# Performance work log

Measured on AMD Instinct MI355X. Metric: run time of the kernel, lower is better.

## Reference

```python
import jax, jax.numpy as jnp
import numpy as np

# Fixed by JastrowNet source: ElectronicSchNet(n_interactions=2, kernel_dim=8, embedding_dim=16, version=1)
BATCH = 512
N_UP, N_DOWN = 16, 16
N_ELEC = N_UP + N_DOWN
N_ATOMS = 8
DIST_FEAT = 32
KERNEL = 8
EMBED = 16
N_LAYERS = 2
W_HIDDEN = 16  # log-spaced hidden dim of the w filter MLP: round(sqrt(32*8))
N_CHAN = 3     # same-spin, anti-spin, nuclear filter channels


def ssp(x):
    # shifted softplus used by SchNet
    return jax.nn.softplus(x) - jnp.log(2.0).astype(x.dtype)


def setup_inputs() -> dict:
    key = jax.random.key(0)
    ks = jax.random.split(key, 16)
    s = lambda fan_in: 1.0 / np.sqrt(fan_in)
    inp = {
        # Gaussian-expanded distance features are non-negative
        'edges_elec': jax.random.uniform(ks[0], (BATCH, N_ELEC, N_ELEC, DIST_FEAT), jnp.float32),
        'edges_nuc': jax.random.uniform(ks[1], (BATCH, N_ELEC, N_ATOMS, DIST_FEAT), jnp.float32),
        # electron spin embedding table (up=0, down=1) and nuclear embeddings Y
        'X_emb': jax.random.normal(ks[2], (2, EMBED), jnp.float32),
        'Y': jax.random.normal(ks[3], (N_ATOMS, KERNEL), jnp.float32),
        # per-layer, per-channel w filter MLP (dist_feat -> hidden -> kernel)
        'wW1': jax.random.normal(ks[4], (N_LAYERS, N_CHAN, DIST_FEAT, W_HIDDEN), jnp.float32) * s(DIST_FEAT),
        'wb1': jnp.zeros((N_LAYERS, N_CHAN, W_HIDDEN), jnp.float32),
        'wW2': jax.random.normal(ks[5], (N_LAYERS, N_CHAN, W_HIDDEN, KERNEL), jnp.float32) * s(W_HIDDEN),
        'wb2': jnp.zeros((N_LAYERS, N_CHAN, KERNEL), jnp.float32),
        # per-layer h subnet (embed -> kernel) and g subnet (kernel -> embed)
        'hW': jax.random.normal(ks[6], (N_LAYERS, EMBED, KERNEL), jnp.float32) * s(EMBED),
        'hb': jnp.zeros((N_LAYERS, KERNEL), jnp.float32),
        'gW': jax.random.normal(ks[7], (N_LAYERS, KERNEL, EMBED), jnp.float32) * s(KERNEL),
        'gb': jnp.zeros((N_LAYERS, EMBED), jnp.float32),
        # readout: Linear(16, 1, bias=False)
        'orb_W': jax.random.normal(ks[8], (EMBED,), jnp.float32) * s(EMBED),
    }
    return inp


def reference(edges_elec, edges_nuc, X_emb, Y, wW1, wb1, wW2, wb2, hW, hb, gW, gb, orb_W):
    B = edges_elec.shape[0]
    spins = jnp.concatenate([jnp.zeros(N_UP, jnp.int32), jnp.ones(N_DOWN, jnp.int32)])
    not_self = ~jnp.eye(N_ELEC, dtype=bool)
    same = ((spins[:, None] == spins[None, :]) & not_self)  # [n,n]
    anti = (spins[:, None] != spins[None, :])

    # initial electron embeddings by spin, broadcast over batch
    x = jnp.broadcast_to(X_emb[spins], (B, N_ELEC, EMBED))

    for l in range(N_LAYERS):
        def w_sub(e, c):
            h1 = ssp(e @ wW1[l, c] + wb1[l, c])
            return ssp(h1 @ wW2[l, c] + wb2[l, c])  # [..., KERNEL]

        w_same = w_sub(edges_elec, 0) * same[None, :, :, None]  # [B,n,n,k]
        w_anti = w_sub(edges_elec, 1) * anti[None, :, :, None]
        w_n = w_sub(edges_nuc, 2)                                # [B,n,m,k]

        hx = ssp(x @ hW[l] + hb[l])                              # [B,n,k]
        # continuous-filter message passing: gather neighbor features, multiply by filter, scatter-sum
        z = jnp.einsum('bijk,bjk->bik', w_same + w_anti, hx)
        z = z + jnp.einsum('bimk,mk->bik', w_n, Y)
        # version 1: single g applied to combined message, residual update
        x = x + z @ gW[l] + gb[l]

    # orbital readout Linear(16,1,bias=False).squeeze(-1).sum(-1)
    return (x @ orb_W).sum(axis=-1)  # [B]
```

## Files before the change

### kernel.cpp

```cpp
#include <hip/hip_runtime.h>
#include <hip/hip_bf16.h>
#include <cstddef>
#include <cstdint>


#define NB   512
#define NE   32
#define NA   8
#define NF   32
#define NH   16
#define NK   8
#define NEMB 16

typedef __attribute__((ext_vector_type(8))) short short8;
typedef __attribute__((ext_vector_type(4))) float f32x4;

__device__ __forceinline__ float ssp(float v){
    return fmaxf(v, 0.f) + __logf(1.f + __expf(-fabsf(v))) - 0.6931471805599453f;
}

__device__ __forceinline__ short f2bf(float x){
    unsigned b = __float_as_uint(x);
    b += 0x7fffu + ((b >> 16) & 1u);
    return (short)(b >> 16);
}
__device__ __forceinline__ unsigned packbf2(float lo, float hi){
    return (unsigned)(unsigned short)f2bf(lo) | ((unsigned)(unsigned short)f2bf(hi) << 16);
}

extern "C" __global__ void __launch_bounds__(256, 4)
filters_kernel(const float* __restrict__ edges_elec,
               const float* __restrict__ edges_nuc,
               const float* __restrict__ X_emb,
               const float* __restrict__ Yk,
               const float* __restrict__ wW1, const float* __restrict__ wb1,
               const float* __restrict__ wW2, const float* __restrict__ wb2,
               const float* __restrict__ hW,  const float* __restrict__ hb,
               __hip_bfloat16* __restrict__ w2out,
               float* __restrict__ z1p,
               float* __restrict__ zn1, float* __restrict__ zn2)
{
    const int bid = blockIdx.x, t = threadIdx.x;
    const int p = bid >> 9, b = bid & 511;
    const bool isNuc = (p == 4);
    const int qi = p >> 1, qj = p & 1;
    const int cc = isNuc ? 2 : ((qi == qj) ? 0 : 1);

    const int lane = t & 63;
    const int r16 = lane & 15, g4 = lane >> 4;
    const int wq = (t >> 6) * 4;

    short8 a1[2], a2[2];
    f32x4 c1[2], c2[2];
#pragma unroll
    for (int l = 0; l < 2; l++){
        const float* W1 = wW1 + (size_t)(l*3 + cc)*NF*NH;
        const float* W2 = wW2 + (size_t)(l*3 + cc)*NH*NK;
        short8 s, s2;
#pragma unroll
        for (int e = 0; e < 8; e++){
            s[e] = f2bf(W1[(g4*8 + e)*NH + r16]);
            const int h = g4*8 + e;
            s2[e] = (h < NH && r16 < NK) ? f2bf(W2[h*NK + r16]) : (short)0;
        }
        a1[l] = s;
        a2[l] = s2;
        const float* B1 = wb1 + (l*3 + cc)*NH;
        const float* B2 = wb2 + (l*3 + cc)*NK;
        f32x4 cb1, cb2;
#pragma unroll
        for (int r = 0; r < 4; r++){
            const int m = g4*4 + r;
            cb1[r] = B1[m];
            cb2[r] = (m < NK) ? B2[m] : 0.f;
        }
        c1[l] = cb1; c2[l] = cb2;
    }

    float hx[4] = {0.f,0.f,0.f,0.f};
    float Yv[4] = {0.f,0.f,0.f,0.f};
    if (!isNuc){
#pragma unroll
        for (int r = 0; r < 4; r++){
            const int kk = (g4*4 + r) & 7;
            float acc = hb[kk];
#pragma unroll
            for (int e = 0; e < NEMB; e++)
                acc = fmaf(X_emb[qj*NEMB + e], hW[e*NK + kk], acc);
            hx[r] = ssp(acc);
        }
    } else {
        const int m = lane & 7;
#pragma unroll
        for (int r = 0; r < 4; r++)
            Yv[r] = Yk[m*NK + ((g4*4 + r) & 7)];
    }

    float4 rawA[4], rawB[4];
    if (!isNuc){
#pragma unroll
        for (int g = 0; g < 4; g++){
            const int i = qi*16 + wq + g;
            const float* src = edges_elec + (((size_t)b*NE + i)*NE + (qj*16 + r16))*NF + g4*8;
            rawA[g] = ((const float4*)src)[0];
            rawB[g] = ((const float4*)src)[1];
        }
    } else {
#pragma unroll
        for (int g = 0; g < 4; g++){
            const int gp = wq + g;
            const int i = 2*gp + (r16 >> 3), m = r16 & 7;
            const float* src = edges_nuc + (((size_t)b*NE + i)*NA + m)*NF + g4*8;
            rawA[g] = ((const float4*)src)[0];
            rawB[g] = ((const float4*)src)[1];
        }
    }
    short8 bfr[4];
#pragma unroll
    for (int g = 0; g < 4; g++){
        short8 s;
        s[0]=f2bf(rawA[g].x); s[1]=f2bf(rawA[g].y); s[2]=f2bf(rawA[g].z); s[3]=f2bf(rawA[g].w);
        s[4]=f2bf(rawB[g].x); s[5]=f2bf(rawB[g].y); s[6]=f2bf(rawB[g].z); s[7]=f2bf(rawB[g].w);
        bfr[g] = s;
    }

    const int s0 = (g4*32 + r16) & 63;
    const int s1 = (g4*32 + 16 + r16) & 63;

#pragma unroll
    for (int g = 0; g < 4; g++){
#pragma unroll
        for (int l = 0; l < 2; l++){
            f32x4 d1 = __builtin_amdgcn_mfma_f32_16x16x32_bf16(a1[l], bfr[g], c1[l], 0, 0, 0);
            const unsigned p0 = packbf2(ssp(d1[0]), ssp(d1[1]));
            const unsigned p1 = packbf2(ssp(d1[2]), ssp(d1[3]));
            unsigned q0 = __shfl(p0, s0, 64);
            unsigned q1 = __shfl(p1, s0, 64);
            unsigned q2 = __shfl(p0, s1, 64);
            unsigned q3 = __shfl(p1, s1, 64);
            if (g4 >= 2){ q0 = 0u; q1 = 0u; q2 = 0u; q3 = 0u; }
            union { unsigned u[4]; short8 v; } bb;
            bb.u[0]=q0; bb.u[1]=q1; bb.u[2]=q2; bb.u[3]=q3;
            f32x4 d2 = __builtin_amdgcn_mfma_f32_16x16x32_bf16(a2[l], bb.v, c2[l], 0, 0, 0);
            float wk[4];
#pragma unroll
            for (int r = 0; r < 4; r++) wk[r] = ssp(d2[r]);

            if (!isNuc){
                const int i16 = wq + g;
                if (cc == 0 && r16 == i16){
#pragma unroll
                    for (int r = 0; r < 4; r++) wk[r] = 0.f;
                }
                if (l == 0){
#pragma unroll
                    for (int off = 1; off < 16; off <<= 1)
#pragma unroll
                        for (int r = 0; r < 4; r++) wk[r] += __shfl_xor(wk[r], off, 64);
                    if (r16 == 0 && g4 < 2){
                        const int i = qi*16 + i16;
                        float4 st;
                        st.x = wk[0]*hx[0]; st.y = wk[1]*hx[1];
                        st.z = wk[2]*hx[2]; st.w = wk[3]*hx[3];
                        *(float4*)&z1p[(((size_t)b*2 + qj)*NE + i)*NK + g4*4] = st;
                    }
                } else if (g4 < 2){
                    const int i = qi*16 + i16, j = qj*16 + r16;
                    uint2 uu;
                    uu.x = packbf2(wk[0], wk[1]);
                    uu.y = packbf2(wk[2], wk[3]);
                    *(uint2*)&w2out[(((size_t)b*NE + i)*NE + j)*NK + g4*4] = uu;
                }
            } else {
#pragma unroll
                for (int r = 0; r < 4; r++) wk[r] *= Yv[r];
#pragma unroll
                for (int off = 1; off < 8; off <<= 1)
#pragma unroll
                    for (int r = 0; r < 4; r++) wk[r] += __shfl_xor(wk[r], off, 64);
                if ((r16 & 7) == 0 && g4 < 2){
                    const int i = 2*(wq + g) + (r16 >> 3);
                    float* dst = (l == 0) ? zn1 : zn2;
                    float4 st; st.x = wk[0]; st.y = wk[1]; st.z = wk[2]; st.w = wk[3];
                    *(float4*)&dst[((size_t)b*NE + i)*NK + g4*4] = st;
                }
            }
        }
    }
}

extern "C" __global__ void __launch_bounds__(256, 4)
update_kernel(const float* __restrict__ X_emb,
              const float* __restrict__ hW,  const float* __restrict__ hb,
              const float* __restrict__ gW,  const float* __restrict__ gb,
              const float* __restrict__ orbW,
              const __hip_bfloat16* __restrict__ w2,
              const float* __restrict__ z1p,
              const float* __restrict__ zn1, const float* __restrict__ zn2,
              float* __restrict__ out)
{
    __shared__ float s_x[NE*NEMB];
    __shared__ float s_z[NE*NK];
    __shared__ float s_hx[NE*NK];
    __shared__ float s_gW[2*NK*NEMB];
    __shared__ float s_gb[2*NEMB];
    __shared__ float s_hW1[NEMB*NK];
    __shared__ float s_hb1[NK];
    __shared__ float s_orb[NEMB];
    __shared__ float s_red[4];

    const int b = blockIdx.x, t = threadIdx.x;

    s_gW[t] = gW[t];
    if (t < 2*NEMB)  s_gb[t]  = gb[t];
    if (t < NEMB*NK) s_hW1[t] = hW[NEMB*NK + t];
    if (t < NK)      s_hb1[t] = hb[NK + t];
    if (t < NEMB)    s_orb[t] = orbW[t];
    {
        const int i = t >> 3, k = t & 7;
        s_z[t] = z1p[(((size_t)b*2 + 0)*NE + i)*NK + k]
               + z1p[(((size_t)b*2 + 1)*NE + i)*NK + k]
               + zn1[((size_t)b*NE + i)*NK + k];
    }
    __syncthreads();
#pragma unroll
    for (int q = 0; q < 2; q++){
        const int idx = q*256 + t, i = idx >> 4, e = idx & 15;
        float acc = s_gb[e];
#pragma unroll
        for (int k = 0; k < NK; k++)
            acc = fmaf(s_z[i*NK + k], s_gW[k*NEMB + e], acc);
        s_x[idx] = X_emb[(i >> 4)*NEMB + e] + acc;
    }
    __syncthreads();
    {
        const int i = t >> 3, k = t & 7;
        float acc = s_hb1[k];
#pragma unroll
        for (int e = 0; e < NEMB; e++)
            acc = fmaf(s_x[i*NEMB + e], s_hW1[e*NK + k], acc);
        s_hx[t] = ssp(acc);
    }
    __syncthreads();
    {
        const int i16 = t >> 4, j16 = t & 15;
#pragma unroll
        for (int qh = 0; qh < 2; qh++){
            const int i = qh*16 + i16;
            float zacc[NK];
#pragma unroll
            for (int k = 0; k < NK; k++) zacc[k] = 0.f;
#pragma unroll
            for (int qj = 0; qj < 2; qj++){
                const int j = qj*16 + j16;
                union { uint4 u; __hip_bfloat16 h[8]; } raw;
                raw.u = *(const uint4*)&w2[((size_t)b*NE*NE + i*NE + j)*NK];
                float pk[NK];
#pragma unroll
                for (int k = 0; k < NK; k++)
                    pk[k] = __bfloat162float(raw.h[k]) * s_hx[j*NK + k];
#pragma unroll
                for (int off = 8; off > 0; off >>= 1)
#pragma unroll
                    for (int k = 0; k < NK; k++) pk[k] += __shfl_down(pk[k], off, 16);
#pragma unroll
                for (int k = 0; k < NK; k++) zacc[k] += pk[k];
            }
            if (j16 == 0){
#pragma unroll
                for (int k = 0; k < NK; k++) s_z[i*NK + k] = zacc[k];
            }
        }
    }
    __syncthreads();
    { const int i = t >> 3, k = t & 7; s_z[t] += zn2[((size_t)b*NE + i)*NK + k]; }
    __syncthreads();
#pragma unroll
    for (int q = 0; q < 2; q++){
        const int idx = q*256 + t, i = idx >> 4, e = idx & 15;
        float acc = s_gb[NEMB + e];
#pragma unroll
        for (int k = 0; k < NK; k++)
            acc = fmaf(s_z[i*NK + k], s_gW[NK*NEMB + k*NEMB + e], acc);
        s_x[idx] += acc;
    }
    __syncthreads();
    float part = (s_x[t] + s_x[t + 256]) * s_orb[t & 15];
#pragma unroll
    for (int off = 32; off > 0; off >>= 1) part += __shfl_down(part, off, 64);
    if ((t & 63) == 0) s_red[t >> 6] = part;
    __syncthreads();
    if (t == 0) out[b] = s_red[0] + s_red[1] + s_red[2] + s_red[3];
}

extern "C" void kernel_launch(void* const* d_in, const int* in_sizes, int n_in,
                              void* d_out, int out_size, void* d_ws, size_t ws_size,
                              hipStream_t stream)
{
    const float* edges_elec = (const float*)d_in[0];
    const float* edges_nuc  = (const float*)d_in[1];
    const float* X_emb      = (const float*)d_in[2];
    const float* Yk         = (const float*)d_in[3];
    const float* wW1        = (const float*)d_in[4];
    const float* wb1        = (const float*)d_in[5];
    const float* wW2        = (const float*)d_in[6];
    const float* wb2        = (const float*)d_in[7];
    const float* hW         = (const float*)d_in[8];
    const float* hb         = (const float*)d_in[9];
    const float* gW         = (const float*)d_in[10];
    const float* gb         = (const float*)d_in[11];
    const float* orbW       = (const float*)d_in[12];

    char* ws = (char*)d_ws;
    __hip_bfloat16* w2 = (__hip_bfloat16*)ws;
    float* z1p = (float*)(ws + 8388608);
    float* zn1 = (float*)(ws + 8388608 + 1048576);
    float* zn2 = (float*)(ws + 8388608 + 1048576 + 524288);

    filters_kernel<<<5*NB, 256, 0, stream>>>(
        edges_elec, edges_nuc, X_emb, Yk, wW1, wb1, wW2, wb2, hW, hb,
        w2, z1p, zn1, zn2);
    update_kernel<<<NB, 256, 0, stream>>>(
        X_emb, hW, hb, gW, gb, orbW, w2, z1p, zn1, zn2, (float*)d_out);
}
```

Baseline: 156.5 us.

## Fuse filter and update kernels into one per-batch kernel using shared memory

Merges the two launches into a single 512-thread block per batch element. The block computes the elec and nuclear filters, keeps the layer-2 bf16 filter tile and the partial messages in LDS, then runs the residual updates and readout. This removes the global workspace round trip for the w2 filter tensor and the second launch. In exchange there are only 512 blocks, each with more serial work and about 24KB of LDS, so there is less parallelism for hiding the latency of the edge loads.

```diff
diff --git a/kernel.cpp b/kernel.cpp
--- a/kernel.cpp
+++ b/kernel.cpp
@@ -27,128 +27,111 @@
 __device__ __forceinline__ unsigned packbf2(float lo, float hi){
     return (unsigned)(unsigned short)f2bf(lo) | ((unsigned)(unsigned short)f2bf(hi) << 16);
 }
-
-extern "C" __global__ void __launch_bounds__(256, 4)
-filters_kernel(const float* __restrict__ edges_elec,
+__device__ __forceinline__ short8 cvt_row(float4 a, float4 b){
+    short8 s;
+    s[0]=f2bf(a.x); s[1]=f2bf(a.y); s[2]=f2bf(a.z); s[3]=f2bf(a.w);
+    s[4]=f2bf(b.x); s[5]=f2bf(b.y); s[6]=f2bf(b.z); s[7]=f2bf(b.w);
+    return s;
+}
+
+extern "C" __global__ void __launch_bounds__(512, 4)
+jastrow_kernel(const float* __restrict__ edges_elec,
                const float* __restrict__ edges_nuc,
                const float* __restrict__ X_emb,
                const float* __restrict__ Yk,
                const float* __restrict__ wW1, const float* __restrict__ wb1,
                const float* __restrict__ wW2, const float* __restrict__ wb2,
                const float* __restrict__ hW,  const float* __restrict__ hb,
-               __hip_bfloat16* __restrict__ w2out,
-               float* __restrict__ z1p,
-               float* __restrict__ zn1, float* __restrict__ zn2)
+               const float* __restrict__ gW,  const float* __restrict__ gb,
+               const float* __restrict__ orbW,
+               float* __restrict__ out)
 {
-    const int bid = blockIdx.x, t = threadIdx.x;
-    const int p = bid >> 9, b = bid & 511;
-    const bool isNuc = (p == 4);
-    const int qi = p >> 1, qj = p & 1;
-    const int cc = isNuc ? 2 : ((qi == qj) ? 0 : 1);
-
-    const int lane = t & 63;
+    __shared__ __align__(16) __hip_bfloat16 s_w2[NE*NE*NK];
+    __shared__ __align__(16) float s_z1p[2*NE*NK];
+    __shared__ __align__(16) float s_zn1[NE*NK];
+    __shared__ __align__(16) float s_zn2[NE*NK];
+    __shared__ float s_hx1[2*NK];
+    __shared__ float s_x[NE*NEMB];
+    __shared__ float s_z[NE*NK];
+    __shared__ float s_hx[NE*NK];
+    __shared__ float s_red[8];
+
+    const int b = blockIdx.x, t = threadIdx.x;
+    const int wid = t >> 6, lane = t & 63;
     const int r16 = lane & 15, g4 = lane >> 4;
-    const int wq = (t >> 6) * 4;
-
-    short8 a1[2], a2[2];
-    f32x4 c1[2], c2[2];
-#pragma unroll
-    for (int l = 0; l < 2; l++){
-        const float* W1 = wW1 + (size_t)(l*3 + cc)*NF*NH;
-        const float* W2 = wW2 + (size_t)(l*3 + cc)*NH*NK;
-        short8 s, s2;
-#pragma unroll
-        for (int e = 0; e < 8; e++){
-            s[e] = f2bf(W1[(g4*8 + e)*NH + r16]);
-            const int h = g4*8 + e;
-            s2[e] = (h < NH && r16 < NK) ? f2bf(W2[h*NK + r16]) : (short)0;
-        }
-        a1[l] = s;
-        a2[l] = s2;
-        const float* B1 = wb1 + (l*3 + cc)*NH;
-        const float* B2 = wb2 + (l*3 + cc)*NK;
-        f32x4 cb1, cb2;
-#pragma unroll
-        for (int r = 0; r < 4; r++){
-            const int m = g4*4 + r;
-            cb1[r] = B1[m];
-            cb2[r] = (m < NK) ? B2[m] : 0.f;
-        }
-        c1[l] = cb1; c2[l] = cb2;
-    }
-
-    float hx[4] = {0.f,0.f,0.f,0.f};
-    float Yv[4] = {0.f,0.f,0.f,0.f};
-    if (!isNuc){
-#pragma unroll
-        for (int r = 0; r < 4; r++){
-            const int kk = (g4*4 + r) & 7;
-            float acc = hb[kk];
-#pragma unroll
-            for (int e = 0; e < NEMB; e++)
-                acc = fmaf(X_emb[qj*NEMB + e], hW[e*NK + kk], acc);
-            hx[r] = ssp(acc);
-        }
-    } else {
-        const int m = lane & 7;
-#pragma unroll
-        for (int r = 0; r < 4; r++)
-            Yv[r] = Yk[m*NK + ((g4*4 + r) & 7)];
-    }
-
-    float4 rawA[4], rawB[4];
-    if (!isNuc){
-#pragma unroll
-        for (int g = 0; g < 4; g++){
-            const int i = qi*16 + wq + g;
-            const float* src = edges_elec + (((size_t)b*NE + i)*NE + (qj*16 + r16))*NF + g4*8;
-            rawA[g] = ((const float4*)src)[0];
-            rawB[g] = ((const float4*)src)[1];
-        }
-    } else {
-#pragma unroll
-        for (int g = 0; g < 4; g++){
-            const int gp = wq + g;
-            const int i = 2*gp + (r16 >> 3), m = r16 & 7;
-            const float* src = edges_nuc + (((size_t)b*NE + i)*NA + m)*NF + g4*8;
-            rawA[g] = ((const float4*)src)[0];
-            rawB[g] = ((const float4*)src)[1];
-        }
-    }
-    short8 bfr[4];
-#pragma unroll
-    for (int g = 0; g < 4; g++){
-        short8 s;
-        s[0]=f2bf(rawA[g].x); s[1]=f2bf(rawA[g].y); s[2]=f2bf(rawA[g].z); s[3]=f2bf(rawA[g].w);
-        s[4]=f2bf(rawB[g].x); s[5]=f2bf(rawB[g].y); s[6]=f2bf(rawB[g].z); s[7]=f2bf(rawB[g].w);
-        bfr[g] = s;
-    }
+
+    if (t < 2*NK){
+        const int s = t >> 3, k = t & 7;
+        float acc = hb[k];
+#pragma unroll
+        for (int e = 0; e < NEMB; e++)
+            acc = fmaf(X_emb[s*NEMB + e], hW[e*NK + k], acc);
+        s_hx1[t] = ssp(acc);
+    }
+    __syncthreads();
 
     const int s0 = (g4*32 + r16) & 63;
     const int s1 = (g4*32 + 16 + r16) & 63;
 
-#pragma unroll
-    for (int g = 0; g < 4; g++){
+    auto build = [&](int cc, short8* a1, short8* a2, f32x4* c1, f32x4* c2){
 #pragma unroll
         for (int l = 0; l < 2; l++){
-            f32x4 d1 = __builtin_amdgcn_mfma_f32_16x16x32_bf16(a1[l], bfr[g], c1[l], 0, 0, 0);
-            const unsigned p0 = packbf2(ssp(d1[0]), ssp(d1[1]));
-            const unsigned p1 = packbf2(ssp(d1[2]), ssp(d1[3]));
-            unsigned q0 = __shfl(p0, s0, 64);
-            unsigned q1 = __shfl(p1, s0, 64);
-            unsigned q2 = __shfl(p0, s1, 64);
-            unsigned q3 = __shfl(p1, s1, 64);
-            if (g4 >= 2){ q0 = 0u; q1 = 0u; q2 = 0u; q3 = 0u; }
-            union { unsigned u[4]; short8 v; } bb;
-            bb.u[0]=q0; bb.u[1]=q1; bb.u[2]=q2; bb.u[3]=q3;
-            f32x4 d2 = __builtin_amdgcn_mfma_f32_16x16x32_bf16(a2[l], bb.v, c2[l], 0, 0, 0);
-            float wk[4];
-#pragma unroll
-            for (int r = 0; r < 4; r++) wk[r] = ssp(d2[r]);
-
-            if (!isNuc){
-                const int i16 = wq + g;
-                if (cc == 0 && r16 == i16){
+            const float* W1 = wW1 + (size_t)(l*3 + cc)*NF*NH;
+            const float* W2 = wW2 + (size_t)(l*3 + cc)*NH*NK;
+            short8 s, s2;
+#pragma unroll
+            for (int e = 0; e < 8; e++){
+                s[e] = f2bf(W1[(g4*8 + e)*NH + r16]);
+                const int h = g4*8 + e;
+                s2[e] = (h < NH && r16 < NK) ? f2bf(W2[h*NK + r16]) : (short)0;
+            }
+            a1[l] = s; a2[l] = s2;
+            const float* B1 = wb1 + (l*3 + cc)*NH;
+            const float* B2 = wb2 + (l*3 + cc)*NK;
+            f32x4 cb1, cb2;
+#pragma unroll
+            for (int r = 0; r < 4; r++){
+                const int m = g4*4 + r;
+                cb1[r] = B1[m];
+                cb2[r] = (m < NK) ? B2[m] : 0.f;
+            }
+            c1[l] = cb1; c2[l] = cb2;
+        }
+    };
+
+#pragma unroll
+    for (int cc = 0; cc < 2; cc++){
+        short8 a1[2], a2[2]; f32x4 c1[2], c2[2];
+        build(cc, a1, a2, c1, c2);
+#pragma unroll
+        for (int u = 0; u < 4; u++){
+            const int tau = wid*4 + u;
+            const int qi = tau >> 4;
+            const int qj = cc ? (1 - qi) : qi;
+            const int g  = tau & 15;
+            const int i  = qi*16 + g;
+            const float* src = edges_elec
+                + (((size_t)b*NE + i)*NE + qj*16 + r16)*NF + g4*8;
+            const float4 ra = ((const float4*)src)[0];
+            const float4 rb = ((const float4*)src)[1];
+            const short8 bfr = cvt_row(ra, rb);
+#pragma unroll
+            for (int l = 0; l < 2; l++){
+                f32x4 d1 = __builtin_amdgcn_mfma_f32_16x16x32_bf16(a1[l], bfr, c1[l], 0, 0, 0);
+                const unsigned p0 = packbf2(ssp(d1[0]), ssp(d1[1]));
+                const unsigned p1 = packbf2(ssp(d1[2]), ssp(d1[3]));
+                unsigned q0 = __shfl(p0, s0, 64);
+                unsigned q1 = __shfl(p1, s0, 64);
+                unsigned q2 = __shfl(p0, s1, 64);
+                unsigned q3 = __shfl(p1, s1, 64);
+                if (g4 >= 2){ q0 = 0u; q1 = 0u; q2 = 0u; q3 = 0u; }
+                union { unsigned u4[4]; short8 v; } bb;
+                bb.u4[0]=q0; bb.u4[1]=q1; bb.u4[2]=q2; bb.u4[3]=q3;
+                f32x4 d2 = __builtin_amdgcn_mfma_f32_16x16x32_bf16(a2[l], bb.v, c2[l], 0, 0, 0);
+                float wk[4];
+#pragma unroll
+                for (int r = 0; r < 4; r++) wk[r] = ssp(d2[r]);
+                if (cc == 0 && r16 == g){
 #pragma unroll
                     for (int r = 0; r < 4; r++) wk[r] = 0.f;
                 }
@@ -158,139 +141,140 @@
 #pragma unroll
                         for (int r = 0; r < 4; r++) wk[r] += __shfl_xor(wk[r], off, 64);
                     if (r16 == 0 && g4 < 2){
-                        const int i = qi*16 + i16;
                         float4 st;
-                        st.x = wk[0]*hx[0]; st.y = wk[1]*hx[1];
-                        st.z = wk[2]*hx[2]; st.w = wk[3]*hx[3];
-                        *(float4*)&z1p[(((size_t)b*2 + qj)*NE + i)*NK + g4*4] = st;
+                        st.x = wk[0]*s_hx1[qj*NK + g4*4 + 0];
+                        st.y = wk[1]*s_hx1[qj*NK + g4*4 + 1];
+                        st.z = wk[2]*s_hx1[qj*NK + g4*4 + 2];
+                        st.w = wk[3]*s_hx1[qj*NK + g4*4 + 3];
+                        *(float4*)&s_z1p[(qj*NE + i)*NK + g4*4] = st;
                     }
                 } else if (g4 < 2){
-                    const int i = qi*16 + i16, j = qj*16 + r16;
+                    const int j = qj*16 + r16;
                     uint2 uu;
                     uu.x = packbf2(wk[0], wk[1]);
                     uu.y = packbf2(wk[2], wk[3]);
-                    *(uint2*)&w2out[(((size_t)b*NE + i)*NE + j)*NK + g4*4] = uu;
+                    *(uint2*)&s_w2[(i*NE + j)*NK + g4*4] = uu;
                 }
-            } else {
-#pragma unroll
-                for (int r = 0; r < 4; r++) wk[r] *= Yv[r];
+            }
+        }
+    }
+
+    {
+        short8 a1[2], a2[2]; f32x4 c1[2], c2[2];
+        build(2, a1, a2, c1, c2);
+        const int m = lane & 7;
+        float Yv[4];
+#pragma unroll
+        for (int r = 0; r < 4; r++)
+            Yv[r] = Yk[m*NK + ((g4*4 + r) & 7)];
+#pragma unroll
+        for (int u = 0; u < 2; u++){
+            const int gp = wid*2 + u;
+            const int i  = 2*gp + (r16 >> 3);
+            const float* src = edges_nuc
+                + (((size_t)b*NE + i)*NA + m)*NF + g4*8;
+            const float4 ra = ((const float4*)src)[0];
+            const float4 rb = ((const float4*)src)[1];
+            const short8 bfr = cvt_row(ra, rb);
+#pragma unroll
+            for (int l = 0; l < 2; l++){
+                f32x4 d1 = __builtin_amdgcn_mfma_f32_16x16x32_bf16(a1[l], bfr, c1[l], 0, 0, 0);
+                const unsigned p0 = packbf2(ssp(d1[0]), ssp(d1[1]));
+                const unsigned p1 = packbf2(ssp(d1[2]), ssp(d1[3]));
+                unsigned q0 = __shfl(p0, s0, 64);
+                unsigned q1 = __shfl(p1, s0, 64);
+                unsigned q2 = __shfl(p0, s1, 64);
+                unsigned q3 = __shfl(p1, s1, 64);
+                if (g4 >= 2){ q0 = 0u; q1 = 0u; q2 = 0u; q3 = 0u; }
+                union { unsigned u4[4]; short8 v; } bb;
+                bb.u4[0]=q0; bb.u4[1]=q1; bb.u4[2]=q2; bb.u4[3]=q3;
+                f32x4 d2 = __builtin_amdgcn_mfma_f32_16x16x32_bf16(a2[l], bb.v, c2[l], 0, 0, 0);
+                float wk[4];
+#pragma unroll
+                for (int r = 0; r < 4; r++) wk[r] = ssp(d2[r]) * Yv[r];
 #pragma unroll
                 for (int off = 1; off < 8; off <<= 1)
 #pragma unroll
                     for (int r = 0; r < 4; r++) wk[r] += __shfl_xor(wk[r], off, 64);
                 if ((r16 & 7) == 0 && g4 < 2){
-                    const int i = 2*(wq + g) + (r16 >> 3);
-                    float* dst = (l == 0) ? zn1 : zn2;
+                    float* dst = l ? s_zn2 : s_zn1;
                     float4 st; st.x = wk[0]; st.y = wk[1]; st.z = wk[2]; st.w = wk[3];
-                    *(float4*)&dst[((size_t)b*NE + i)*NK + g4*4] = st;
+                    *(float4*)&dst[i*NK + g4*4] = st;
                 }
             }
         }
     }
-}
-
-extern "C" __global__ void __launch_bounds__(256, 4)
-update_kernel(const float* __restrict__ X_emb,
-              const float* __restrict__ hW,  const float* __restrict__ hb,
-              const float* __restrict__ gW,  const float* __restrict__ gb,
-              const float* __restrict__ orbW,
-              const __hip_bfloat16* __restrict__ w2,
-              const float* __restrict__ z1p,
-              const float* __restrict__ zn1, const float* __restrict__ zn2,
-              float* __restrict__ out)
-{
-    __shared__ float s_x[NE*NEMB];
-    __shared__ float s_z[NE*NK];
-    __shared__ float s_hx[NE*NK];
-    __shared__ float s_gW[2*NK*NEMB];
-    __shared__ float s_gb[2*NEMB];
-    __shared__ float s_hW1[NEMB*NK];
-    __shared__ float s_hb1[NK];
-    __shared__ float s_orb[NEMB];
-    __shared__ float s_red[4];
-
-    const int b = blockIdx.x, t = threadIdx.x;
-
-    s_gW[t] = gW[t];
-    if (t < 2*NEMB)  s_gb[t]  = gb[t];
-    if (t < NEMB*NK) s_hW1[t] = hW[NEMB*NK + t];
-    if (t < NK)      s_hb1[t] = hb[NK + t];
-    if (t < NEMB)    s_orb[t] = orbW[t];
+    __syncthreads();
+
+    if (t < NE*NK)
+        s_z[t] = s_z1p[t] + s_z1p[NE*NK + t] + s_zn1[t];
+    __syncthreads();
     {
+        const int i = t >> 4, e = t & 15;
+        float acc = gb[e];
+#pragma unroll
+        for (int k = 0; k < NK; k++)
+            acc = fmaf(s_z[i*NK + k], gW[k*NEMB + e], acc);
+        s_x[t] = X_emb[(i >> 4)*NEMB + e] + acc;
+    }
+    __syncthreads();
+    if (t < NE*NK){
         const int i = t >> 3, k = t & 7;
-        s_z[t] = z1p[(((size_t)b*2 + 0)*NE + i)*NK + k]
-               + z1p[(((size_t)b*2 + 1)*NE + i)*NK + k]
-               + zn1[((size_t)b*NE + i)*NK + k];
-    }
-    __syncthreads();
-#pragma unroll
-    for (int q = 0; q < 2; q++){
-        const int idx = q*256 + t, i = idx >> 4, e = idx & 15;
-        float acc = s_gb[e];
+        float acc = hb[NK + k];
+#pragma unroll
+        for (int e = 0; e < NEMB; e++)
+            acc = fmaf(s_x[i*NEMB + e], hW[NEMB*NK + e*NK + k], acc);
+        s_hx[t] = ssp(acc);
+    }
+    __syncthreads();
+    {
+        const int i = t >> 4, j16 = t & 15;
+        float zacc[NK];
+#pragma unroll
+        for (int k = 0; k < NK; k++) zacc[k] = 0.f;
+#pragma unroll
+        for (int qj = 0; qj < 2; qj++){
+            const int j = qj*16 + j16;
+            union { uint4 u; __hip_bfloat16 h[8]; } raw;
+            raw.u = *(const uint4*)&s_w2[((size_t)i*NE + j)*NK];
+            float pk[NK];
+#pragma unroll
+            for (int k = 0; k < NK; k++)
+                pk[k] = __bfloat162float(raw.h[k]) * s_hx[j*NK + k];
+#pragma unroll
+            for (int off = 8; off > 0; off >>= 1)
+#pragma unroll
+                for (int k = 0; k < NK; k++) pk[k] += __shfl_down(pk[k], off, 16);
+#pragma unroll
+            for (int k = 0; k < NK; k++) zacc[k] += pk[k];
+        }
+        if (j16 == 0){
+#pragma unroll
+            for (int k = 0; k < NK; k++)
+                s_z[i*NK + k] = zacc[k] + s_zn2[i*NK + k];
+        }
+    }
+    __syncthreads();
+    {
+        const int i = t >> 4, e = t & 15;
+        float acc = gb[NEMB + e];
 #pragma unroll
         for (int k = 0; k < NK; k++)
-            acc = fmaf(s_z[i*NK + k], s_gW[k*NEMB + e], acc);
-        s_x[idx] = X_emb[(i >> 4)*NEMB + e] + acc;
-    }
-    __syncthreads();
-    {
-        const int i = t >> 3, k = t & 7;
-        float acc = s_hb1[k];
-#pragma unroll
-        for (int e = 0; e < NEMB; e++)
-            acc = fmaf(s_x[i*NEMB + e], s_hW1[e*NK + k], acc);
-        s_hx[t] = ssp(acc);
-    }
-    __syncthreads();
-    {
-        const int i16 = t >> 4, j16 = t & 15;
-#pragma unroll
-        for (int qh = 0; qh < 2; qh++){
-            const int i = qh*16 + i16;
-            float zacc[NK];
-#pragma unroll
-            for (int k = 0; k < NK; k++) zacc[k] = 0.f;
-#pragma unroll
-            for (int qj = 0; qj < 2; qj++){
-                const int j = qj*16 + j16;
-                union { uint4 u; __hip_bfloat16 h[8]; } raw;
-                raw.u = *(const uint4*)&w2[((size_t)b*NE*NE + i*NE + j)*NK];
-                float pk[NK];
-#pragma unroll
-                for (int k = 0; k < NK; k++)
-                    pk[k] = __bfloat162float(raw.h[k]) * s_hx[j*NK + k];
-#pragma unroll
-                for (int off = 8; off > 0; off >>= 1)
-#pragma unroll
-                    for (int k = 0; k < NK; k++) pk[k] += __shfl_down(pk[k], off, 16);
-#pragma unroll
-                for (int k = 0; k < NK; k++) zacc[k] += pk[k];
-            }
-            if (j16 == 0){
-#pragma unroll
-                for (int k = 0; k < NK; k++) s_z[i*NK + k] = zacc[k];
-            }
-        }
-    }
-    __syncthreads();
-    { const int i = t >> 3, k = t & 7; s_z[t] += zn2[((size_t)b*NE + i)*NK + k]; }
-    __syncthreads();
-#pragma unroll
-    for (int q = 0; q < 2; q++){
-        const int idx = q*256 + t, i = idx >> 4, e = idx & 15;
-        float acc = s_gb[NEMB + e];
-#pragma unroll
-        for (int k = 0; k < NK; k++)
-            acc = fmaf(s_z[i*NK + k], s_gW[NK*NEMB + k*NEMB + e], acc);
-        s_x[idx] += acc;
-    }
-    __syncthreads();
-    float part = (s_x[t] + s_x[t + 256]) * s_orb[t & 15];
+            acc = fmaf(s_z[i*NK + k], gW[NK*NEMB + k*NEMB + e], acc);
+        s_x[t] += acc;
+    }
+    __syncthreads();
+    float part = s_x[t] * orbW[t & 15];
 #pragma unroll
     for (int off = 32; off > 0; off >>= 1) part += __shfl_down(part, off, 64);
-    if ((t & 63) == 0) s_red[t >> 6] = part;
-    __syncthreads();
-    if (t == 0) out[b] = s_red[0] + s_red[1] + s_red[2] + s_red[3];
+    if (lane == 0) s_red[wid] = part;
+    __syncthreads();
+    if (t == 0){
+        float r = 0.f;
+#pragma unroll
+        for (int w = 0; w < 8; w++) r += s_red[w];
+        out[b] = r;
+    }
 }
 
 extern "C" void kernel_launch(void* const* d_in, const int* in_sizes, int n_in,
@@ -311,15 +295,7 @@
     const float* gb         = (const float*)d_in[11];
     const float* orbW       = (const float*)d_in[12];
 
-    char* ws = (char*)d_ws;
-    __hip_bfloat16* w2 = (__hip_bfloat16*)ws;
-    float* z1p = (float*)(ws + 8388608);
-    float* zn1 = (float*)(ws + 8388608 + 1048576);
-    float* zn2 = (float*)(ws + 8388608 + 1048576 + 524288);
-
-    filters_kernel<<<5*NB, 256, 0, stream>>>(
+    jastrow_kernel<<<NB, 512, 0, stream>>>(
         edges_elec, edges_nuc, X_emb, Yk, wW1, wb1, wW2, wb2, hW, hb,
-        w2, z1p, zn1, zn2);
-    update_kernel<<<NB, 256, 0, stream>>>(
-        X_emb, hW, hb, gW, gb, orbW, w2, z1p, zn1, zn2, (float*)d_out);
-}
+        gW, gb, orbW, (float*)d_out);
+}
```

Measured after the change: 156.2 us. Within noise of the previous version (-0.2%).
